# Performance work log

Hardware: AMD Instinct MI355X
Metric: run time of the kernel (lower is better)

Reference implementation:

```python
import jax, jax.numpy as jnp
import numpy as np

N_HEAD, D_MODEL, D_K, D_V = 16, 1024, 64, 64
BIAS_WEIGHT = 1.0
NEG = -10000.0


def setup_inputs() -> dict:
    key = jax.random.key(0)
    ks = jax.random.split(key, 9)
    B, L = 2, 2048
    q = jax.random.normal(ks[0], (B, L, D_MODEL), dtype=jnp.float32)
    k = jax.random.normal(ks[1], (B, L, D_MODEL), dtype=jnp.float32)
    v = jax.random.normal(ks[2], (B, L, D_MODEL), dtype=jnp.float32)
    mask = jax.random.randint(ks[3], (B, L, L), 0, 2, dtype=jnp.int32)
    bias = jax.random.normal(ks[4], (B, L, L), dtype=jnp.float32)
    s = 1.0 / np.sqrt(D_MODEL)
    w_qs = jax.random.uniform(ks[5], (D_MODEL, N_HEAD * D_K), jnp.float32, -s, s)
    w_ks = jax.random.uniform(ks[6], (D_MODEL, N_HEAD * D_K), jnp.float32, -s, s)
    w_vs = jax.random.uniform(ks[7], (D_MODEL, N_HEAD * D_V), jnp.float32, -s, s)
    w_fc = jax.random.uniform(ks[8], (N_HEAD * D_V, D_MODEL), jnp.float32, -s, s)
    return {"q": q, "k": k, "v": v, "mask": mask, "bias": bias,
            "w_qs": w_qs, "w_ks": w_ks, "w_vs": w_vs, "w_fc": w_fc}


def reference(q, k, v, mask, bias, w_qs, w_ks, w_vs, w_fc):
    B, Lq, _ = q.shape
    # project and split heads: [B, H, L, d]
    qh = (q @ w_qs).reshape(B, Lq, N_HEAD, D_K).transpose(0, 2, 1, 3)
    kh = (k @ w_ks).reshape(B, k.shape[1], N_HEAD, D_K).transpose(0, 2, 1, 3)
    vh = (v @ w_vs).reshape(B, v.shape[1], N_HEAD, D_V).transpose(0, 2, 1, 3)
    temperature = D_K ** 0.5
    attn = jnp.einsum('bhqd,bhkd->bhqk', qh / temperature, kh)
    attn = attn + bias[:, None, :, :] * BIAS_WEIGHT
    attn = jnp.where(mask[:, None, :, :] == 0, NEG, attn)
    attn = jax.nn.softmax(attn, axis=-1)
    out = jnp.einsum('bhqk,bhkd->bhqd', attn, vh)
    out = out.transpose(0, 2, 1, 3).reshape(B, Lq, N_HEAD * D_V)
    return out @ w_fc
```

## Files before the change

### kernel.cpp

```cpp
#include <hip/hip_runtime.h>
#include <cstddef>

#define DEV static __device__ __forceinline__

typedef float f32x4 __attribute__((ext_vector_type(4)));
typedef __bf16 bf16x8 __attribute__((ext_vector_type(8)));
typedef __bf16 bf16x4v __attribute__((ext_vector_type(4)));
typedef unsigned short u16x8 __attribute__((ext_vector_type(8)));
typedef unsigned short u16x4 __attribute__((ext_vector_type(4)));
typedef unsigned u32x2 __attribute__((ext_vector_type(2)));
typedef unsigned u32x4 __attribute__((ext_vector_type(4)));
typedef _Float16 f16;
typedef _Float16 f16x4 __attribute__((ext_vector_type(4)));

constexpr int BB = 2, LL = 2048, DM = 1024, NH = 16, DK = 64;
constexpr float LOG2E = 1.44269504f;

DEV unsigned short f2bf(float f) {
  unsigned u = __builtin_bit_cast(unsigned, f);
  u += 0x7fffu + ((u >> 16) & 1u);
  return (unsigned short)(u >> 16);
}
DEV u16x4 cvt4(f32x4 v) {
  bf16x4v b = __builtin_convertvector(v, bf16x4v);
  return __builtin_bit_cast(u16x4, b);
}
DEV bf16x8 asbf(u16x8 v) { return __builtin_bit_cast(bf16x8, v); }
DEV f32x4 mfma16(u16x8 a, u16x8 b, f32x4 c) {
  return __builtin_amdgcn_mfma_f32_16x16x32_bf16(asbf(a), asbf(b), c, 0, 0, 0);
}
#if __has_builtin(__builtin_amdgcn_exp2f)
DEV float fexp2(float x) { return __builtin_amdgcn_exp2f(x); }
#else
DEV float fexp2(float x) { return exp2f(x); }
#endif
DEV void swap32(unsigned& a, unsigned& b) {
#if __has_builtin(__builtin_amdgcn_permlane32_swap)
  u32x2 r = __builtin_amdgcn_permlane32_swap(a, b, false, false);
  a = r[0]; b = r[1];
#else
  asm("v_permlane32_swap_b32 %0, %1" : "+v"(a), "+v"(b));
#endif
}
DEV void swap16(unsigned& a, unsigned& b) {
#if __has_builtin(__builtin_amdgcn_permlane16_swap)
  u32x2 r = __builtin_amdgcn_permlane16_swap(a, b, false, false);
  a = r[0]; b = r[1];
#else
  asm("v_permlane16_swap_b32 %0, %1" : "+v"(a), "+v"(b));
#endif
}
DEV void g2lds16(const void* g, void* l) {
  __builtin_amdgcn_global_load_lds(
      (const __attribute__((address_space(1))) unsigned int*)g,
      (__attribute__((address_space(3))) unsigned int*)l, 16, 0, 0);
}

__global__ __launch_bounds__(256) void prep_all(
    const float* __restrict__ w0, const float* __restrict__ w1,
    const float* __restrict__ w2, const float* __restrict__ w3,
    unsigned short* __restrict__ wT, const int* __restrict__ mask,
    const float* __restrict__ bias, f16* __restrict__ bmf,
    const float* __restrict__ s0, const float* __restrict__ s1,
    const float* __restrict__ s2, unsigned short* __restrict__ qkvb) {
  int f = blockIdx.x, t = threadIdx.x;
  if (f < 4096) {
    __shared__ float tile[32][33];
    int z = f >> 10, rem = f & 1023;
    int k0 = (rem >> 5) * 32, n0 = (rem & 31) * 32;
    const float* W = (z == 0) ? w0 : (z == 1) ? w1 : (z == 2) ? w2 : w3;
    unsigned short* out = wT + (size_t)z * DM * DM;
    int tx = t & 31, ty = t >> 5;
#pragma unroll
    for (int p = 0; p < 4; p++)
      tile[ty + 8 * p][tx] = W[(size_t)(k0 + ty + 8 * p) * DM + n0 + tx];
    __syncthreads();
#pragma unroll
    for (int p = 0; p < 4; p++)
      out[(size_t)(n0 + ty + 8 * p) * DM + k0 + tx] = f2bf(tile[tx][ty + 8 * p]);
  } else if (f < 12288) {
    int f2 = f - 4096;
    int w = t >> 6, lane = t & 63;
    int bq = f2 >> 5;
    int kt = (f2 & 31) * 4 + w;
    int b = bq >> 7, qt = bq & 127;
    int q = qt * 16 + (lane & 15);
    int k = kt * 16 + (lane >> 4) * 4;
    size_t src = ((size_t)b * LL + q) * LL + k;
    int4 mk = *(const int4*)(mask + src);
    float4 bs = *(const float4*)(bias + src);
    f16x4 o;
    o[0] = (f16)((mk.x == 0 ? -10000.f : bs.x) * LOG2E);
    o[1] = (f16)((mk.y == 0 ? -10000.f : bs.y) * LOG2E);
    o[2] = (f16)((mk.z == 0 ? -10000.f : bs.z) * LOG2E);
    o[3] = (f16)((mk.w == 0 ? -10000.f : bs.w) * LOG2E);
    *(f16x4*)(bmf + ((size_t)bq * 128 + kt) * 256 + lane * 4) = o;
  } else {
    int f3 = f - 12288;
    int z = f3 >> 11;
    const float* src = (z == 0) ? s0 : (z == 1) ? s1 : s2;
    size_t i = ((size_t)(f3 & 2047) * 256 + t) * 8;
    float4 a = *(const float4*)(src + i);
    float4 b = *(const float4*)(src + i + 4);
    u16x8 o;
    o[0] = f2bf(a.x); o[1] = f2bf(a.y); o[2] = f2bf(a.z); o[3] = f2bf(a.w);
    o[4] = f2bf(b.x); o[5] = f2bf(b.y); o[6] = f2bf(b.z); o[7] = f2bf(b.w);
    *(u16x8*)(qkvb + (size_t)z * (size_t)(BB * LL) * DM + i) = o;
  }
}

template <int KITERS>
DEV void gemm_core(const unsigned short* __restrict__ A,
                   const unsigned short* __restrict__ BT,
                   unsigned short* Al, unsigned short* Bl,
                   int m0, int n0, int k0beg, int t, f32x4 (&acc)[4][4]) {
  int lane = t & 63, c = lane & 15, qd = lane >> 4;
  int w = t >> 6, wm = w >> 1, wn = w & 1;
  int r0 = t >> 3;
  int gsw = (t & 7) ^ (r0 & 7);

#pragma unroll 1
  for (int kk = 0; kk < KITERS; ++kk) {
    int k0 = k0beg + kk * 64;
#pragma unroll
    for (int p = 0; p < 4; ++p) {
      g2lds16(&A[(size_t)(m0 + 32 * p + r0) * DM + k0 + 8 * gsw],
              &Al[p * 2048 + w * 512]);
      g2lds16(&BT[(size_t)(n0 + 32 * p + r0) * DM + k0 + 8 * gsw],
              &Bl[p * 2048 + w * 512]);
    }
    __syncthreads();
#pragma unroll
    for (int ks = 0; ks < 2; ++ks) {
      u16x8 af[4], bfr[4];
#pragma unroll
      for (int mt = 0; mt < 4; ++mt)
        af[mt] = *(const u16x8*)&Al[(64 * wm + 16 * mt + c) * 64 +
                                    (((4 * ks + qd) ^ (c & 7)) << 3)];
#pragma unroll
      for (int nt = 0; nt < 4; ++nt)
        bfr[nt] = *(const u16x8*)&Bl[(64 * wn + 16 * nt + c) * 64 +
                                     (((4 * ks + qd) ^ (c & 7)) << 3)];
#pragma unroll
      for (int mt = 0; mt < 4; ++mt)
#pragma unroll
        for (int nt = 0; nt < 4; ++nt)
          acc[mt][nt] = mfma16(af[mt], bfr[nt], acc[mt][nt]);
    }
    __syncthreads();
  }
}

__global__ __launch_bounds__(256, 3) void proj_gemm(
    const unsigned short* __restrict__ qkvb, const unsigned short* __restrict__ wT,
    unsigned short* __restrict__ qh, unsigned short* __restrict__ kh,
    unsigned short* __restrict__ vT) {
  __shared__ unsigned short Al[128 * 64];
  __shared__ unsigned short Bl[128 * 64];
  int o = blockIdx.x;
  int wg = (o & 7) * 96 + (o >> 3);
  int z = wg >> 8, rem = wg & 255;
  int m0 = (rem >> 3) * 128, n0 = (rem & 7) * 128;
  const unsigned short* A = qkvb + (size_t)z * BB * LL * DM;
  const unsigned short* BT = wT + (size_t)z * DM * DM;
  int t = threadIdx.x, lane = t & 63, c = lane & 15, qd = lane >> 4;
  int w = t >> 6, wm = w >> 1, wn = w & 1;
  f32x4 acc[4][4] = {};
  gemm_core<DM / 64>(A, BT, Al, Bl, m0, n0, 0, t, acc);

  if (z == 2) {
#pragma unroll
    for (int mt = 0; mt < 4; ++mt)
#pragma unroll
      for (int nt = 0; nt < 4; ++nt) {
        int n = n0 + 64 * wn + 16 * nt + c;
        int h = n >> 6, d = n & 63;
        int m = m0 + 64 * wm + 16 * mt + 4 * qd;
        int b = m >> 11, l = m & 2047;
        *(u16x4*)&vT[(((size_t)b * NH + h) * DK + d) * LL + l] = cvt4(acc[mt][nt]);
      }
  } else {
    unsigned short* Ch = z ? kh : qh;
    float scale = z ? 1.0f : 0.125f * LOG2E;
#pragma unroll
    for (int mt = 0; mt < 4; ++mt)
#pragma unroll
      for (int nt = 0; nt < 4; ++nt) {
        int n = n0 + 64 * wn + 16 * nt + c;
        int h = n >> 6, d = n & 63;
#pragma unroll
        for (int i = 0; i < 4; ++i) {
          int m = m0 + 64 * wm + 16 * mt + 4 * qd + i;
          int b = m >> 11, l = m & 2047;
          Ch[(((size_t)b * NH + h) * LL + l) * DK + d] = f2bf(acc[mt][nt][i] * scale);
        }
      }
  }
}

__global__ __launch_bounds__(256, 3) void fc_gemm(const unsigned short* __restrict__ A,
                                                  const unsigned short* __restrict__ BT,
                                                  float* __restrict__ C) {
  __shared__ unsigned short Al[128 * 64];
  __shared__ unsigned short Bl[128 * 64];
  int o = blockIdx.x;
  int wg = (o & 7) * 32 + (o >> 3);
  int m0 = (wg >> 3) * 128, n0 = (wg & 7) * 128;
  int t = threadIdx.x, lane = t & 63, c = lane & 15, qd = lane >> 4;
  int w = t >> 6, wm = w >> 1, wn = w & 1;
  f32x4 acc[4][4] = {};
  gemm_core<DM / 64>(A, BT, Al, Bl, m0, n0, 0, t, acc);
#pragma unroll
  for (int mt = 0; mt < 4; ++mt)
#pragma unroll
    for (int nt = 0; nt < 4; ++nt) {
      int n = n0 + 64 * wn + 16 * nt + c;
#pragma unroll
      for (int i = 0; i < 4; ++i) {
        int m = m0 + 64 * wm + 16 * mt + 4 * qd + i;
        C[(size_t)m * DM + n] = acc[mt][nt][i];
      }
    }
}

__global__ __launch_bounds__(128, 2) void attn_kern(
    const unsigned short* __restrict__ qh, const unsigned short* __restrict__ kh,
    const unsigned short* __restrict__ vT, const f16* __restrict__ bmf,
    unsigned short* __restrict__ O) {
  __shared__ unsigned short Kb[2][4096];
  __shared__ unsigned short Vb[2][4096];

  int t = threadIdx.x, w = t >> 6, lane = t & 63, c = lane & 15, qd = lane >> 4;
  int o = blockIdx.x;
  int wg = (o & 7) * 128 + (o >> 3);
  int x = wg & 31, h = (wg >> 5) & 15, b = wg >> 9;
  int q0 = x * 64;
  const unsigned short* Q = qh + (((size_t)b * NH + h) * LL + q0) * DK;
  const unsigned short* K = kh + ((size_t)b * NH + h) * LL * DK;
  const unsigned short* V = vT + ((size_t)b * NH + h) * DK * LL;
  const f16* BMF0 = bmf + (((size_t)b * 128 + x * 4 + 2 * w) * 128) * 256 + lane * 4;
  const f16* BMF1 = BMF0 + (size_t)128 * 256;
  int rt = t >> 3, gg = t & 7;

#pragma unroll
  for (int r = 0; r < 4; ++r) {
    int row = r * 16 + rt;
    int sc = ((gg ^ (row & 7)) << 3);
    g2lds16(&Q[(size_t)row * DK + sc], &Kb[1][r * 1024 + w * 512]);
    g2lds16(&K[(size_t)row * DK + sc], &Kb[0][r * 1024 + w * 512]);
    g2lds16(&V[(size_t)row * LL + sc], &Vb[0][r * 1024 + w * 512]);
  }
  f16x4 bA[8], bB[8];
#pragma unroll
  for (int nt = 0; nt < 2; ++nt)
#pragma unroll
    for (int mt = 0; mt < 4; ++mt)
      bA[nt * 4 + mt] = *(const f16x4*)((nt ? BMF1 : BMF0) + (size_t)mt * 256);
  __syncthreads();

  u16x8 qf[2][2];
#pragma unroll
  for (int nt = 0; nt < 2; ++nt)
#pragma unroll
    for (int ks = 0; ks < 2; ++ks)
      qf[nt][ks] = *(const u16x8*)&Kb[1][(32 * w + 16 * nt + c) * 64 +
                                         (((4 * ks + qd) ^ (c & 7)) << 3)];
  __syncthreads();

  const u16x8 ones = {0x3F80, 0x3F80, 0x3F80, 0x3F80,
                      0x3F80, 0x3F80, 0x3F80, 0x3F80};
  f32x4 lacc[2] = {};
  f32x4 oacc[4][2] = {};

  auto body = [&](int it, f16x4 (&bc)[8], f16x4 (&bn)[8]) {
    int cur = it & 1;
    const unsigned short* Kl = Kb[cur];
    const unsigned short* Vt = Vb[cur];
    if (it + 1 < 32) {
      int nb = cur ^ 1, kt1 = (it + 1) * 64;
#pragma unroll
      for (int r = 0; r < 4; ++r) {
        int row = r * 16 + rt;
        int sc = ((gg ^ (row & 7)) << 3);
        g2lds16(&K[(size_t)(kt1 + row) * DK + sc], &Kb[nb][r * 1024 + w * 512]);
        g2lds16(&V[(size_t)row * LL + kt1 + sc], &Vb[nb][r * 1024 + w * 512]);
      }
#pragma unroll
      for (int nt = 0; nt < 2; ++nt)
#pragma unroll
        for (int mt = 0; mt < 4; ++mt)
          bn[nt * 4 + mt] = *(const f16x4*)((nt ? BMF1 : BMF0) +
                                            (size_t)((it + 1) * 4 + mt) * 256);
    }

    f32x4 s[4][2];
    __builtin_amdgcn_s_setprio(1);
#pragma unroll
    for (int mt = 0; mt < 4; ++mt) {
      int row = 16 * mt + c;
      u16x8 k0f = *(const u16x8*)&Kl[row * 64 + ((qd ^ (c & 7)) << 3)];
      u16x8 k1f = *(const u16x8*)&Kl[row * 64 + (((4 + qd) ^ (c & 7)) << 3)];
#pragma unroll
      for (int nt = 0; nt < 2; ++nt) {
        f16x4 b4 = bc[nt * 4 + mt];
        f32x4 z = {(float)b4[0], (float)b4[1], (float)b4[2], (float)b4[3]};
        z = mfma16(k0f, qf[nt][0], z);
        s[mt][nt] = mfma16(k1f, qf[nt][1], z);
      }
    }
    __builtin_amdgcn_s_setprio(0);
    u16x8 pf[2][2];
#pragma unroll
    for (int nt = 0; nt < 2; ++nt) {
      unsigned L[4], H[4];
#pragma unroll
      for (int mt = 0; mt < 4; ++mt) {
        f32x4 p;
#pragma unroll
        for (int i = 0; i < 4; ++i) p[i] = fexp2(s[mt][nt][i]);
        u32x2 lw = __builtin_bit_cast(u32x2, cvt4(p));
        L[mt] = lw[0];
        H[mt] = lw[1];
      }
#pragma unroll
      for (int ks = 0; ks < 2; ++ks) {
        unsigned l0 = L[2 * ks], l1 = L[2 * ks + 1];
        unsigned h0 = H[2 * ks], h1 = H[2 * ks + 1];
        swap32(l0, l1); swap16(l0, l1);
        swap32(h0, h1); swap16(h0, h1);
        u32x4 pw = {l0, h0, l1, h1};
        pf[nt][ks] = __builtin_bit_cast(u16x8, pw);
      }
    }
    __builtin_amdgcn_s_setprio(1);
#pragma unroll
    for (int nt = 0; nt < 2; ++nt) {
      lacc[nt] = mfma16(ones, pf[nt][0], lacc[nt]);
      lacc[nt] = mfma16(ones, pf[nt][1], lacc[nt]);
    }
#pragma unroll
    for (int dt = 0; dt < 4; ++dt) {
      int row = 16 * dt + c;
      u16x8 v0f = *(const u16x8*)&Vt[row * 64 + ((qd ^ (c & 7)) << 3)];
      u16x8 v1f = *(const u16x8*)&Vt[row * 64 + (((4 + qd) ^ (c & 7)) << 3)];
#pragma unroll
      for (int nt = 0; nt < 2; ++nt) {
        oacc[dt][nt] = mfma16(v0f, pf[nt][0], oacc[dt][nt]);
        oacc[dt][nt] = mfma16(v1f, pf[nt][1], oacc[dt][nt]);
      }
    }
    __builtin_amdgcn_s_setprio(0);
    __syncthreads();
  };

#pragma unroll 1
  for (int it = 0; it < 32; it += 2) {
    body(it, bA, bB);
    body(it + 1, bB, bA);
  }

#pragma unroll
  for (int nt = 0; nt < 2; ++nt) {
    float rl = 1.f / lacc[nt][0];
    size_t orow = ((size_t)b * LL + q0 + 32 * w + 16 * nt + c) * DM + h * DK;
#pragma unroll
    for (int dt = 0; dt < 4; ++dt)
      *(u16x4*)&O[orow + 16 * dt + 4 * qd] = cvt4(oacc[dt][nt] * rl);
  }
}

extern "C" void kernel_launch(void* const* d_in, const int* in_sizes, int n_in,
                              void* d_out, int out_size, void* d_ws, size_t ws_size,
                              hipStream_t stream) {
  (void)in_sizes; (void)n_in; (void)ws_size; (void)out_size;
  const float* q = (const float*)d_in[0];
  const float* k = (const float*)d_in[1];
  const float* v = (const float*)d_in[2];
  const int* mask = (const int*)d_in[3];
  const float* bias = (const float*)d_in[4];
  const float* w_qs = (const float*)d_in[5];
  const float* w_ks = (const float*)d_in[6];
  const float* w_vs = (const float*)d_in[7];
  const float* w_fc = (const float*)d_in[8];

  char* ws = (char*)d_ws;
  const size_t MB = 1024 * 1024;
  unsigned short* wT = (unsigned short*)(ws);
  f16* bmf = (f16*)(ws + 8 * MB);
  unsigned short* qkvb = (unsigned short*)(ws + 24 * MB);
  unsigned short* qh = (unsigned short*)(ws + 48 * MB);
  unsigned short* kh = (unsigned short*)(ws + 56 * MB);
  unsigned short* vhT = (unsigned short*)(ws + 64 * MB);
  unsigned short* Obuf = (unsigned short*)(ws + 72 * MB);

  prep_all<<<dim3(18432), dim3(256), 0, stream>>>(w_qs, w_ks, w_vs, w_fc, wT,
                                                  mask, bias, bmf, q, k, v, qkvb);
  proj_gemm<<<dim3(768), 256, 0, stream>>>(qkvb, wT, qh, kh, vhT);
  attn_kern<<<dim3(1024), dim3(128), 0, stream>>>(qh, kh, vhT, bmf, Obuf);
  fc_gemm<<<dim3(256), 256, 0, stream>>>(Obuf, wT + (size_t)3 * DM * DM,
                                         (float*)d_out);
}
```

Measured before the change: 270.9 us.

## Load attention K/V fragments directly from global into registers, drop LDS staging

After: 353.0 us. 30.3% more time.

```diff
diff --git a/kernel.cpp b/kernel.cpp
--- a/kernel.cpp
+++ b/kernel.cpp
@@ -223,98 +223,77 @@
     }
 }
 
-__global__ __launch_bounds__(128, 2) void attn_kern(
+__global__ __launch_bounds__(256, 2) void attn_kern(
     const unsigned short* __restrict__ qh, const unsigned short* __restrict__ kh,
     const unsigned short* __restrict__ vT, const f16* __restrict__ bmf,
     unsigned short* __restrict__ O) {
-  __shared__ unsigned short Kb[2][4096];
-  __shared__ unsigned short Vb[2][4096];
-
   int t = threadIdx.x, w = t >> 6, lane = t & 63, c = lane & 15, qd = lane >> 4;
   int o = blockIdx.x;
-  int wg = (o & 7) * 128 + (o >> 3);
-  int x = wg & 31, h = (wg >> 5) & 15, b = wg >> 9;
-  int q0 = x * 64;
+  int wg = (o & 7) * 64 + (o >> 3);
+  int x = wg & 15, h = (wg >> 4) & 15, b = wg >> 8;
+  int q0 = x * 128;
   const unsigned short* Q = qh + (((size_t)b * NH + h) * LL + q0) * DK;
   const unsigned short* K = kh + ((size_t)b * NH + h) * LL * DK;
   const unsigned short* V = vT + ((size_t)b * NH + h) * DK * LL;
-  const f16* BMF0 = bmf + (((size_t)b * 128 + x * 4 + 2 * w) * 128) * 256 + lane * 4;
+  const f16* BMF0 = bmf + (((size_t)b * 128 + x * 8 + 2 * w) * 128) * 256 + lane * 4;
   const f16* BMF1 = BMF0 + (size_t)128 * 256;
-  int rt = t >> 3, gg = t & 7;
-
-#pragma unroll
-  for (int r = 0; r < 4; ++r) {
-    int row = r * 16 + rt;
-    int sc = ((gg ^ (row & 7)) << 3);
-    g2lds16(&Q[(size_t)row * DK + sc], &Kb[1][r * 1024 + w * 512]);
-    g2lds16(&K[(size_t)row * DK + sc], &Kb[0][r * 1024 + w * 512]);
-    g2lds16(&V[(size_t)row * LL + sc], &Vb[0][r * 1024 + w * 512]);
-  }
-  f16x4 bA[8], bB[8];
+
+  u16x8 qf[2][2];
 #pragma unroll
   for (int nt = 0; nt < 2; ++nt)
 #pragma unroll
-    for (int mt = 0; mt < 4; ++mt)
-      bA[nt * 4 + mt] = *(const f16x4*)((nt ? BMF1 : BMF0) + (size_t)mt * 256);
-  __syncthreads();
-
-  u16x8 qf[2][2];
-#pragma unroll
-  for (int nt = 0; nt < 2; ++nt)
-#pragma unroll
     for (int ks = 0; ks < 2; ++ks)
-      qf[nt][ks] = *(const u16x8*)&Kb[1][(32 * w + 16 * nt + c) * 64 +
-                                         (((4 * ks + qd) ^ (c & 7)) << 3)];
-  __syncthreads();
+      qf[nt][ks] =
+          *(const u16x8*)&Q[(size_t)(32 * w + 16 * nt + c) * DK + 8 * (4 * ks + qd)];
 
   const u16x8 ones = {0x3F80, 0x3F80, 0x3F80, 0x3F80,
                       0x3F80, 0x3F80, 0x3F80, 0x3F80};
   f32x4 lacc[2] = {};
   f32x4 oacc[4][2] = {};
 
-  auto body = [&](int it, f16x4 (&bc)[8], f16x4 (&bn)[8]) {
-    int cur = it & 1;
-    const unsigned short* Kl = Kb[cur];
-    const unsigned short* Vt = Vb[cur];
-    if (it + 1 < 32) {
-      int nb = cur ^ 1, kt1 = (it + 1) * 64;
-#pragma unroll
-      for (int r = 0; r < 4; ++r) {
-        int row = r * 16 + rt;
-        int sc = ((gg ^ (row & 7)) << 3);
-        g2lds16(&K[(size_t)(kt1 + row) * DK + sc], &Kb[nb][r * 1024 + w * 512]);
-        g2lds16(&V[(size_t)row * LL + kt1 + sc], &Vb[nb][r * 1024 + w * 512]);
-      }
-#pragma unroll
-      for (int nt = 0; nt < 2; ++nt)
-#pragma unroll
-        for (int mt = 0; mt < 4; ++mt)
-          bn[nt * 4 + mt] = *(const f16x4*)((nt ? BMF1 : BMF0) +
-                                            (size_t)((it + 1) * 4 + mt) * 256);
-    }
-
-    f32x4 s[4][2];
+  u16x8 kfA[4], vfA[4], kfB[4], vfB[4];
+  f16x4 bA[4], bB[4];
+
+  auto loadset = [&](int it, u16x8 (&kf)[4], u16x8 (&vf)[4], f16x4 (&bb)[4]) {
+    const unsigned short* Kt = K + (size_t)it * 32 * DK;
+    const unsigned short* Vt = V + (size_t)it * 32;
+#pragma unroll
+    for (int mt = 0; mt < 2; ++mt)
+#pragma unroll
+      for (int ks = 0; ks < 2; ++ks)
+        kf[mt * 2 + ks] =
+            *(const u16x8*)&Kt[(size_t)(16 * mt + c) * DK + 8 * (4 * ks + qd)];
+#pragma unroll
+    for (int dt = 0; dt < 4; ++dt)
+      vf[dt] = *(const u16x8*)&Vt[(size_t)(16 * dt + c) * LL + 8 * qd];
+#pragma unroll
+    for (int nt = 0; nt < 2; ++nt)
+#pragma unroll
+      for (int mt = 0; mt < 2; ++mt)
+        bb[nt * 2 + mt] =
+            *(const f16x4*)((nt ? BMF1 : BMF0) + (size_t)(it * 2 + mt) * 256);
+  };
+
+  auto compute = [&](const u16x8 (&kf)[4], const u16x8 (&vf)[4],
+                     const f16x4 (&bb)[4]) {
+    f32x4 s[2][2];
     __builtin_amdgcn_s_setprio(1);
 #pragma unroll
-    for (int mt = 0; mt < 4; ++mt) {
-      int row = 16 * mt + c;
-      u16x8 k0f = *(const u16x8*)&Kl[row * 64 + ((qd ^ (c & 7)) << 3)];
-      u16x8 k1f = *(const u16x8*)&Kl[row * 64 + (((4 + qd) ^ (c & 7)) << 3)];
+    for (int mt = 0; mt < 2; ++mt)
 #pragma unroll
       for (int nt = 0; nt < 2; ++nt) {
-        f16x4 b4 = bc[nt * 4 + mt];
+        f16x4 b4 = bb[nt * 2 + mt];
         f32x4 z = {(float)b4[0], (float)b4[1], (float)b4[2], (float)b4[3]};
-        z = mfma16(k0f, qf[nt][0], z);
-        s[mt][nt] = mfma16(k1f, qf[nt][1], z);
-      }
-    }
+        z = mfma16(kf[mt * 2 + 0], qf[nt][0], z);
+        s[mt][nt] = mfma16(kf[mt * 2 + 1], qf[nt][1], z);
+      }
     __builtin_amdgcn_s_setprio(0);
-    u16x8 pf[2][2];
+    u16x8 pf[2];
 #pragma unroll
     for (int nt = 0; nt < 2; ++nt) {
-      unsigned L[4], H[4];
-#pragma unroll
-      for (int mt = 0; mt < 4; ++mt) {
+      unsigned L[2], H[2];
+#pragma unroll
+      for (int mt = 0; mt < 2; ++mt) {
         f32x4 p;
 #pragma unroll
         for (int i = 0; i < 4; ++i) p[i] = fexp2(s[mt][nt][i]);
@@ -322,41 +301,30 @@
         L[mt] = lw[0];
         H[mt] = lw[1];
       }
-#pragma unroll
-      for (int ks = 0; ks < 2; ++ks) {
-        unsigned l0 = L[2 * ks], l1 = L[2 * ks + 1];
-        unsigned h0 = H[2 * ks], h1 = H[2 * ks + 1];
-        swap32(l0, l1); swap16(l0, l1);
-        swap32(h0, h1); swap16(h0, h1);
-        u32x4 pw = {l0, h0, l1, h1};
-        pf[nt][ks] = __builtin_bit_cast(u16x8, pw);
-      }
+      unsigned l0 = L[0], l1 = L[1], h0 = H[0], h1 = H[1];
+      swap32(l0, l1); swap16(l0, l1);
+      swap32(h0, h1); swap16(h0, h1);
+      u32x4 pw = {l0, h0, l1, h1};
+      pf[nt] = __builtin_bit_cast(u16x8, pw);
     }
     __builtin_amdgcn_s_setprio(1);
 #pragma unroll
-    for (int nt = 0; nt < 2; ++nt) {
-      lacc[nt] = mfma16(ones, pf[nt][0], lacc[nt]);
-      lacc[nt] = mfma16(ones, pf[nt][1], lacc[nt]);
-    }
-#pragma unroll
-    for (int dt = 0; dt < 4; ++dt) {
-      int row = 16 * dt + c;
-      u16x8 v0f = *(const u16x8*)&Vt[row * 64 + ((qd ^ (c & 7)) << 3)];
-      u16x8 v1f = *(const u16x8*)&Vt[row * 64 + (((4 + qd) ^ (c & 7)) << 3)];
-#pragma unroll
-      for (int nt = 0; nt < 2; ++nt) {
-        oacc[dt][nt] = mfma16(v0f, pf[nt][0], oacc[dt][nt]);
-        oacc[dt][nt] = mfma16(v1f, pf[nt][1], oacc[dt][nt]);
-      }
-    }
+    for (int nt = 0; nt < 2; ++nt) lacc[nt] = mfma16(ones, pf[nt], lacc[nt]);
+#pragma unroll
+    for (int dt = 0; dt < 4; ++dt)
+#pragma unroll
+      for (int nt = 0; nt < 2; ++nt)
+        oacc[dt][nt] = mfma16(vf[dt], pf[nt], oacc[dt][nt]);
     __builtin_amdgcn_s_setprio(0);
-    __syncthreads();
   };
 
+  loadset(0, kfA, vfA, bA);
 #pragma unroll 1
-  for (int it = 0; it < 32; it += 2) {
-    body(it, bA, bB);
-    body(it + 1, bB, bA);
+  for (int it = 0; it < 64; it += 2) {
+    loadset(it + 1, kfB, vfB, bB);
+    compute(kfA, vfA, bA);
+    if (it + 2 < 64) loadset(it + 2, kfA, vfA, bA);
+    compute(kfB, vfB, bB);
   }
 
 #pragma unroll
@@ -396,7 +364,7 @@
   prep_all<<<dim3(18432), dim3(256), 0, stream>>>(w_qs, w_ks, w_vs, w_fc, wT,
                                                   mask, bias, bmf, q, k, v, qkvb);
   proj_gemm<<<dim3(768), 256, 0, stream>>>(qkvb, wT, qh, kh, vhT);
-  attn_kern<<<dim3(1024), dim3(128), 0, stream>>>(qh, kh, vhT, bmf, Obuf);
+  attn_kern<<<dim3(512), dim3(256), 0, stream>>>(qh, kh, vhT, bmf, Obuf);
   fc_gemm<<<dim3(256), 256, 0, stream>>>(Obuf, wT + (size_t)3 * DM * DM,
                                          (float*)d_out);
 }
```
